# Kernel tuning notes

Hardware: AMD Instinct MI355X
Metric: run time of the kernel (lower is better)

Reference implementation:

```python
import jax, jax.numpy as jnp
import numpy as np

NUM_HEADS = 16
D_MODEL = 1024
HEAD_DIM = D_MODEL // NUM_HEADS
B, S = 2, 2048


def setup_inputs() -> dict:
    key = jax.random.key(0)
    ks = jax.random.split(key, 11)
    scale = 1.0 / np.sqrt(D_MODEL)
    inp = {
        'query': jax.random.normal(ks[0], (B, S, D_MODEL), jnp.float32),
        'key': jax.random.normal(ks[1], (B, S, D_MODEL), jnp.float32),
        'value': jax.random.normal(ks[2], (B, S, D_MODEL), jnp.float32),
        'Wq': jax.random.normal(ks[3], (D_MODEL, D_MODEL), jnp.float32) * scale,
        'bq': jnp.zeros((D_MODEL,), jnp.float32),
        'Wk': jax.random.normal(ks[4], (D_MODEL, D_MODEL), jnp.float32) * scale,
        'bk': jnp.zeros((D_MODEL,), jnp.float32),
        'Wv': jax.random.normal(ks[5], (D_MODEL, D_MODEL), jnp.float32) * scale,
        'bv': jnp.zeros((D_MODEL,), jnp.float32),
        'Wo': jax.random.normal(ks[6], (D_MODEL, D_MODEL), jnp.float32) * scale,
        'bo': jnp.zeros((D_MODEL,), jnp.float32),
    }
    return inp


def reference(query, key, value, Wq, bq, Wk, bk, Wv, bv, Wo, bo):
    b, s, _ = query.shape
    # Linear projections (torch Linear: x @ W.T + b; here W stored as [in,out])
    Q = query @ Wq + bq
    K = key @ Wk + bk
    V = value @ Wv + bv
    # [B, H, S, Dh]
    Q = Q.reshape(b, s, NUM_HEADS, HEAD_DIM).transpose(0, 2, 1, 3)
    K = K.reshape(b, -1, NUM_HEADS, HEAD_DIM).transpose(0, 2, 1, 3)
    V = V.reshape(b, -1, NUM_HEADS, HEAD_DIM).transpose(0, 2, 1, 3)
    scores = jnp.einsum('bhqd,bhkd->bhqk', Q, K) / jnp.sqrt(jnp.float32(HEAD_DIM)).astype(Q.dtype)
    attn = jax.nn.softmax(scores, axis=-1)
    ctx = jnp.einsum('bhqk,bhkd->bhqd', attn, V)
    ctx = ctx.transpose(0, 2, 1, 3).reshape(b, s, D_MODEL)
    return ctx @ Wo + bo
```

## Files before the change

kernel.cpp:

```cpp
#include <hip/hip_runtime.h>
#include <hip/hip_bf16.h>
#include <math.h>

#define NUM_HEADS 16
#define D_MODEL 1024
#define HEAD_DIM 64
#define BATCH 2
#define SEQ 2048
#define M_TOTAL (BATCH*SEQ)

typedef __bf16 bf16;
typedef __bf16 bf16x2 __attribute__((ext_vector_type(2)));
typedef __bf16 bf16x4 __attribute__((ext_vector_type(4)));
typedef __bf16 bf16x8 __attribute__((ext_vector_type(8)));
typedef float  floatx4  __attribute__((ext_vector_type(4)));
typedef float  floatx16 __attribute__((ext_vector_type(16)));
typedef unsigned int uintx2 __attribute__((ext_vector_type(2)));
typedef unsigned int uintx4 __attribute__((ext_vector_type(4)));

#define CLSCALE 0.180336884f

#if __has_builtin(__builtin_amdgcn_exp2f)
#define EXP2(x) __builtin_amdgcn_exp2f(x)
#else
#define EXP2(x) exp2f(x)
#endif

__device__ __forceinline__ void async_copy16(const bf16* g, bf16* l) {
    __builtin_amdgcn_global_load_lds(
        (const __attribute__((address_space(1))) void*)g,
        (__attribute__((address_space(3))) void*)l, 16, 0, 0);
}

__device__ __forceinline__ unsigned pk2(float lo, float hi) {
    bf16x2 t; t[0] = (bf16)lo; t[1] = (bf16)hi;
    return __builtin_bit_cast(unsigned, t);
}

__global__ __launch_bounds__(256)
void convert_kernel(const float* __restrict__ Wq, const float* __restrict__ Wk,
                    const float* __restrict__ Wv, const float* __restrict__ Wo,
                    const float* __restrict__ q, const float* __restrict__ k,
                    const float* __restrict__ v,
                    bf16* __restrict__ Wt, bf16* __restrict__ Xb)
{
    const int blk = blockIdx.x;
    const int tid = threadIdx.x;
    if (blk < 256) {
        const int wi  = blk >> 6;
        const int sub = blk & 63;
        const int xb  = sub & 3;
        const int yb  = sub >> 2;
        const float* W = (wi == 0) ? Wq : (wi == 1) ? Wk : (wi == 2) ? Wv : Wo;
        bf16* dstM = Wt + (size_t)wi * D_MODEL * D_MODEL;
        const int n  = xb * 256 + tid;
        const int k0 = yb * 64;
        bf16* dst = dstM + (size_t)n * D_MODEL + k0;
        #pragma unroll
        for (int jc = 0; jc < 8; ++jc) {
            bf16x8 w;
            #pragma unroll
            for (int j = 0; j < 8; ++j)
                w[j] = (bf16)W[(size_t)(k0 + jc * 8 + j) * D_MODEL + n];
            *(bf16x8*)(dst + jc * 8) = w;
        }
    } else {
        const int rem   = blk - 256;
        const int plane = rem >> 11;
        const int xb    = rem & 2047;
        const float* X = (plane == 0) ? q : (plane == 1) ? k : v;
        bf16* dst = Xb + (size_t)plane * M_TOTAL * D_MODEL;
        size_t i = ((size_t)xb * 256 + tid) * 8;
        const float4 u = *(const float4*)(X + i);
        const float4 w = *(const float4*)(X + i + 4);
        bf16x8 o;
        o[0] = (bf16)u.x; o[1] = (bf16)u.y; o[2] = (bf16)u.z; o[3] = (bf16)u.w;
        o[4] = (bf16)w.x; o[5] = (bf16)w.y; o[6] = (bf16)w.z; o[7] = (bf16)w.w;
        *(bf16x8*)(dst + i) = o;
    }
}

__global__ __launch_bounds__(256)
void proj_kernel(const bf16* __restrict__ Xb, const bf16* __restrict__ Wt,
                 const float* __restrict__ bq, const float* __restrict__ bk,
                 const float* __restrict__ bv,
                 bf16* __restrict__ Qo, bf16* __restrict__ Ko, bf16* __restrict__ Vto)
{
    const int lin  = blockIdx.x;
    const int xcd  = lin & 7;
    const int idx  = lin >> 3;
    const int nt   = idx & 7;
    const int t2   = idx >> 3;
    const int mloc = t2 & 3;
    const int which= t2 >> 2;
    const int tileM = (xcd * 4 + mloc) * 128;
    const int tileN = nt * 128;

    const bf16* X     = Xb + (size_t)which * M_TOTAL * D_MODEL;
    const bf16* Wm    = Wt + (size_t)which * D_MODEL * D_MODEL;
    const float* bias = (which == 0) ? bq : (which == 1) ? bk : bv;

    const int tid  = threadIdx.x;
    const int lane = tid & 63;
    const int wave = tid >> 6;
    const int quad = lane >> 4;
    const int l16  = lane & 15;

    __shared__ bf16 sA[128 * 32];
    __shared__ bf16 sB[128 * 32];

    floatx4 acc[4][4];
    const floatx4 z4 = {0.0f, 0.0f, 0.0f, 0.0f};
    #pragma unroll
    for (int i = 0; i < 4; i++)
        #pragma unroll
        for (int j = 0; j < 4; j++) acc[i][j] = z4;

    const int wm = (wave >> 1) * 64;
    const int wn = (wave & 1) * 64;

    const int c0   = wave * 64 + lane;
    const int row0 = c0 >> 2, col0 = (c0 & 3) * 8;
    const int c1   = c0 + 256;
    const int row1 = c1 >> 2, col1 = (c1 & 3) * 8;
    bf16* ldsA0 = sA + (size_t)(wave * 64) * 8;
    bf16* ldsA1 = sA + (size_t)(256 + wave * 64) * 8;
    bf16* ldsB0 = sB + (size_t)(wave * 64) * 8;
    bf16* ldsB1 = sB + (size_t)(256 + wave * 64) * 8;

    for (int k0 = 0; k0 < D_MODEL; k0 += 32) {
        __syncthreads();
        async_copy16(X  + (size_t)(tileM + row0) * D_MODEL + k0 + col0, ldsA0);
        async_copy16(X  + (size_t)(tileM + row1) * D_MODEL + k0 + col1, ldsA1);
        async_copy16(Wm + (size_t)(tileN + row0) * D_MODEL + k0 + col0, ldsB0);
        async_copy16(Wm + (size_t)(tileN + row1) * D_MODEL + k0 + col1, ldsB1);
        __syncthreads();

        bf16x8 af[4], bfr[4];
        #pragma unroll
        for (int i = 0; i < 4; i++) af[i]  = *(const bf16x8*)&sA[(wm + i * 16 + l16) * 32 + quad * 8];
        #pragma unroll
        for (int j = 0; j < 4; j++) bfr[j] = *(const bf16x8*)&sB[(wn + j * 16 + l16) * 32 + quad * 8];
        if (which != 2) {
            #pragma unroll
            for (int i = 0; i < 4; i++)
                #pragma unroll
                for (int j = 0; j < 4; j++)
                    acc[i][j] = __builtin_amdgcn_mfma_f32_16x16x32_bf16(af[i], bfr[j], acc[i][j], 0, 0, 0);
        } else {
            #pragma unroll
            for (int i = 0; i < 4; i++)
                #pragma unroll
                for (int j = 0; j < 4; j++)
                    acc[i][j] = __builtin_amdgcn_mfma_f32_16x16x32_bf16(bfr[i], af[j], acc[i][j], 0, 0, 0);
        }
    }

    if (which != 2) {
        bf16* out = (which == 0) ? Qo : Ko;
        const float oscale = (which == 0) ? CLSCALE : 1.0f;
        #pragma unroll
        for (int i = 0; i < 4; i++) {
            int mbase = tileM + wm + i * 16 + quad * 4;
            #pragma unroll
            for (int j = 0; j < 4; j++) {
                int n = tileN + wn + j * 16 + l16;
                float bb = bias[n];
                int h = n >> 6, d = n & 63;
                #pragma unroll
                for (int r = 0; r < 4; r++) {
                    int mm = mbase + r;
                    int b = mm >> 11, s = mm & 2047;
                    out[(((size_t)(b * NUM_HEADS + h)) * SEQ + s) * HEAD_DIM + d] =
                        (bf16)((acc[i][j][r] + bb) * oscale);
                }
            }
        }
    } else {
        #pragma unroll
        for (int i = 0; i < 4; i++) {
            #pragma unroll
            for (int r = 0; r < 4; r++) {
                int n = tileN + wn + i * 16 + quad * 4 + r;
                float bb = bias[n];
                int h = n >> 6, d = n & 63;
                #pragma unroll
                for (int j = 0; j < 4; j++) {
                    int m = tileM + wm + j * 16 + l16;
                    int b = m >> 11, s = m & 2047;
                    Vto[(((size_t)(b * NUM_HEADS + h)) * HEAD_DIM + d) * SEQ + s] =
                        (bf16)(acc[i][j][r] + bb);
                }
            }
        }
    }
}

__global__ __launch_bounds__(256)
void attn_kernel(const bf16* __restrict__ Q, const bf16* __restrict__ K,
                 const bf16* __restrict__ Vt, bf16* __restrict__ Ctx)
{
    const int lin    = blockIdx.x;
    const int xcd    = lin & 7;
    const int rest   = lin >> 3;
    const int superg = rest >> 5;
    const int qi     = rest & 31;
    const int bh     = superg * 8 + xcd;
    const int b      = bh >> 4, h = bh & 15;
    const int q0     = qi * 64;

    const int tid  = threadIdx.x;
    const int lane = tid & 63;
    const int wave = tid >> 6;
    const int half = lane >> 5;
    const int m31  = lane & 31;
    const int xs   = m31 & 7;

    const int qsub  = wave & 1;
    const int kjsub = wave >> 1;

    __shared__ bf16 sK[2][64 * 64];
    __shared__ bf16 sV[2][64 * 64];
    __shared__ float sL[64];

    const bf16* Qb  = Q  + ((size_t)bh * SEQ + q0) * HEAD_DIM;
    const bf16* Kb  = K  + (size_t)bh * SEQ * HEAD_DIM;
    const bf16* Vtb = Vt + (size_t)bh * HEAD_DIM * SEQ;

    bf16x8 bQ[4];
    #pragma unroll
    for (int s = 0; s < 4; s++)
        bQ[s] = *(const bf16x8*)(Qb + (size_t)(qsub * 32 + m31) * HEAD_DIM + s * 16 + half * 8);

    #pragma unroll
    for (int it = 0; it < 2; ++it) {
        int c    = tid + it * 256;
        int row  = c >> 3;
        int scol = ((c & 7) ^ (row & 7)) * 8;
        async_copy16(Kb  + (size_t)row * HEAD_DIM + scol, &sK[0][c * 8]);
        async_copy16(Vtb + (size_t)row * SEQ + scol,      &sV[0][c * 8]);
    }

    floatx16 o0, o1;
    #pragma unroll
    for (int r = 0; r < 16; r++) { o0[r] = 0.0f; o1[r] = 0.0f; }
    float lp = 0.0f;

    for (int kt = 0; kt < SEQ / 64; ++kt) {
        const int p = kt & 1;
        __syncthreads();

        bf16x8 aK[4];
        #pragma unroll
        for (int s = 0; s < 4; s++)
            aK[s] = *(const bf16x8*)&sK[p][(kjsub * 32 + m31) * 64 + (((2 * s + half) ^ xs) * 8)];

        if (kt + 1 < SEQ / 64) {
            #pragma unroll
            for (int it = 0; it < 2; ++it) {
                int c    = tid + it * 256;
                int row  = c >> 3;
                int scol = ((c & 7) ^ (row & 7)) * 8;
                async_copy16(Kb  + (size_t)((kt + 1) * 64 + row) * HEAD_DIM + scol,
                             &sK[p ^ 1][c * 8]);
                async_copy16(Vtb + (size_t)row * SEQ + (kt + 1) * 64 + scol,
                             &sV[p ^ 1][c * 8]);
            }
        }

        floatx16 sc;
        #pragma unroll
        for (int r = 0; r < 16; r++) sc[r] = 0.0f;
        __builtin_amdgcn_s_setprio(1);
        #pragma unroll
        for (int s = 0; s < 4; s++)
            sc = __builtin_amdgcn_mfma_f32_32x32x16_bf16(aK[s], bQ[s], sc, 0, 0, 0);
        __builtin_amdgcn_s_setprio(0);

        #pragma unroll
        for (int r = 0; r < 16; r++) sc[r] = EXP2(sc[r]);
        float ls = 0.0f;
        #pragma unroll
        for (int r = 0; r < 16; r++) ls += sc[r];
        lp += ls;

        bf16x8 bP[2];
        #pragma unroll
        for (int s = 0; s < 2; s++) {
            const int bs = 8 * s;
            unsigned x = pk2(sc[bs + 0], sc[bs + 1]);
            unsigned z = pk2(sc[bs + 2], sc[bs + 3]);
            unsigned y = pk2(sc[bs + 4], sc[bs + 5]);
            unsigned w = pk2(sc[bs + 6], sc[bs + 7]);
            auto r0 = __builtin_amdgcn_permlane32_swap(x, y, false, false);
            auto r1 = __builtin_amdgcn_permlane32_swap(z, w, false, false);
            uintx4 bp;
            bp[0] = r0[0]; bp[1] = r1[0]; bp[2] = r0[1]; bp[3] = r1[1];
            bP[s] = __builtin_bit_cast(bf16x8, bp);
        }

        __builtin_amdgcn_s_setprio(1);
        #pragma unroll
        for (int s = 0; s < 2; s++) {
            int ch = ((4 * kjsub + 2 * s + half) ^ xs) * 8;
            bf16x8 a0 = *(const bf16x8*)&sV[p][(size_t)m31 * 64 + ch];
            bf16x8 a1 = *(const bf16x8*)&sV[p][(size_t)(32 + m31) * 64 + ch];
            o0 = __builtin_amdgcn_mfma_f32_32x32x16_bf16(a0, bP[s], o0, 0, 0, 0);
            o1 = __builtin_amdgcn_mfma_f32_32x32x16_bf16(a1, bP[s], o1, 0, 0, 0);
        }
        __builtin_amdgcn_s_setprio(0);
    }

    lp += __shfl_xor(lp, 32, 64);

    __syncthreads();
    float* fO = (qsub == 0) ? (float*)&sK[0][0] : (float*)&sK[1][0];
    if (kjsub == 1) {
        #pragma unroll
        for (int r = 0; r < 16; r++) {
            fO[r * 64 + lane]        = o0[r];
            fO[1024 + r * 64 + lane] = o1[r];
        }
        if (half == 0) sL[qsub * 32 + m31] = lp;
    }
    __syncthreads();
    if (kjsub == 0) {
        #pragma unroll
        for (int r = 0; r < 16; r++) {
            o0[r] += fO[r * 64 + lane];
            o1[r] += fO[1024 + r * 64 + lane];
        }
        float denom = lp + sL[qsub * 32 + m31];
        float inv = 1.0f / denom;

        int q = q0 + qsub * 32 + m31;
        size_t base = ((size_t)b * SEQ + q) * D_MODEL + h * HEAD_DIM;
        #pragma unroll
        for (int rg = 0; rg < 4; rg++) {
            int d0 = rg * 8 + half * 4;
            bf16x4 w0, w1;
            #pragma unroll
            for (int i = 0; i < 4; i++) {
                w0[i] = (bf16)(o0[rg * 4 + i] * inv);
                w1[i] = (bf16)(o1[rg * 4 + i] * inv);
            }
            *(bf16x4*)&Ctx[base + d0]      = w0;
            *(bf16x4*)&Ctx[base + 32 + d0] = w1;
        }
    }
}

__global__ __launch_bounds__(256)
void out_proj_kernel(const bf16* __restrict__ A, const bf16* __restrict__ Wto,
                     const float* __restrict__ bias, float* __restrict__ Out)
{
    const int lin  = blockIdx.x;
    const int xcd  = lin & 7;
    const int idx  = lin >> 3;
    const int nt   = idx & 7;
    const int mloc = idx >> 3;
    const int tileM = (xcd * 8 + mloc) * 64;
    const int tileN = nt * 128;

    const int tid  = threadIdx.x;
    const int lane = tid & 63;
    const int wave = tid >> 6;
    const int quad = lane >> 4;
    const int l16  = lane & 15;

    __shared__ bf16 sA[64 * 32];
    __shared__ bf16 sB[128 * 32];

    floatx4 acc[2][4];
    const floatx4 z4 = {0.0f, 0.0f, 0.0f, 0.0f};
    #pragma unroll
    for (int i = 0; i < 2; i++)
        #pragma unroll
        for (int j = 0; j < 4; j++) acc[i][j] = z4;

    const int wm = (wave >> 1) * 32;
    const int wn = (wave & 1) * 64;

    const int c0   = wave * 64 + lane;
    const int row0 = c0 >> 2, col0 = (c0 & 3) * 8;
    const int c1   = c0 + 256;
    const int row1 = c1 >> 2, col1 = (c1 & 3) * 8;
    bf16* ldsA0 = sA + (size_t)(wave * 64) * 8;
    bf16* ldsB0 = sB + (size_t)(wave * 64) * 8;
    bf16* ldsB1 = sB + (size_t)(256 + wave * 64) * 8;

    for (int k0 = 0; k0 < D_MODEL; k0 += 32) {
        __syncthreads();
        async_copy16(A   + (size_t)(tileM + row0) * D_MODEL + k0 + col0, ldsA0);
        async_copy16(Wto + (size_t)(tileN + row0) * D_MODEL + k0 + col0, ldsB0);
        async_copy16(Wto + (size_t)(tileN + row1) * D_MODEL + k0 + col1, ldsB1);
        __syncthreads();

        bf16x8 af[2], bfr[4];
        #pragma unroll
        for (int i = 0; i < 2; i++) af[i]  = *(const bf16x8*)&sA[(wm + i * 16 + l16) * 32 + quad * 8];
        #pragma unroll
        for (int j = 0; j < 4; j++) bfr[j] = *(const bf16x8*)&sB[(wn + j * 16 + l16) * 32 + quad * 8];
        #pragma unroll
        for (int i = 0; i < 2; i++)
            #pragma unroll
            for (int j = 0; j < 4; j++)
                acc[i][j] = __builtin_amdgcn_mfma_f32_16x16x32_bf16(af[i], bfr[j], acc[i][j], 0, 0, 0);
    }

    #pragma unroll
    for (int i = 0; i < 2; i++) {
        int mbase = tileM + wm + i * 16 + quad * 4;
        #pragma unroll
        for (int j = 0; j < 4; j++) {
            int n = tileN + wn + j * 16 + l16;
            float bb = bias[n];
            #pragma unroll
            for (int r = 0; r < 4; r++)
                Out[(size_t)(mbase + r) * D_MODEL + n] = acc[i][j][r] + bb;
        }
    }
}

extern "C" void kernel_launch(void* const* d_in, const int* in_sizes, int n_in,
                              void* d_out, int out_size, void* d_ws, size_t ws_size,
                              hipStream_t stream)
{
    const float* q  = (const float*)d_in[0];
    const float* k  = (const float*)d_in[1];
    const float* v  = (const float*)d_in[2];
    const float* Wq = (const float*)d_in[3];
    const float* bq = (const float*)d_in[4];
    const float* Wk = (const float*)d_in[5];
    const float* bk = (const float*)d_in[6];
    const float* Wv = (const float*)d_in[7];
    const float* bv = (const float*)d_in[8];
    const float* Wo = (const float*)d_in[9];
    const float* bo = (const float*)d_in[10];
    float* out = (float*)d_out;

    const size_t PLANE = (size_t)M_TOTAL * D_MODEL;
    bf16* Qb = (bf16*)d_ws;
    bf16* Kb = Qb + PLANE;
    bf16* Vt = Kb + PLANE;
    bf16* Cb = Vt + PLANE;
    bf16* Wt = Cb + PLANE;
    bf16* Xb = Wt + 4 * (size_t)D_MODEL * D_MODEL;

    convert_kernel<<<dim3(6400), 256, 0, stream>>>(Wq, Wk, Wv, Wo, q, k, v, Wt, Xb);
    proj_kernel<<<dim3(768), 256, 0, stream>>>(Xb, Wt, bq, bk, bv, Qb, Kb, Vt);
    attn_kernel<<<dim3(1024), 256, 0, stream>>>(Qb, Kb, Vt, Cb);
    out_proj_kernel<<<dim3(512), 256, 0, stream>>>(Cb, Wt + 3 * (size_t)D_MODEL * D_MODEL, bo, out);
}
```

Before: 236.9 us.

## Double-buffer LDS tiles and use fragment-ordered layout in projection GEMMs

Both the QKV projection kernel and the output projection kernel now use two LDS buffers. The next K-slice is prefetched with async copies while MFMAs run on the current slice, which removes one barrier per iteration and overlaps global loads with compute. The LDS tiles are also stored in fragment order, so each lane reads 16 contiguous bytes and bank conflicts are avoided. In exchange, LDS use per block doubles, which may reduce occupancy.

Result: slower. 254.4 us (+7.4%).

```diff
diff --git a/kernel.cpp b/kernel.cpp
--- a/kernel.cpp
+++ b/kernel.cpp
@@ -106,8 +106,8 @@
     const int quad = lane >> 4;
     const int l16  = lane & 15;
 
-    __shared__ bf16 sA[128 * 32];
-    __shared__ bf16 sB[128 * 32];
+    __shared__ bf16 sA[2][4096];
+    __shared__ bf16 sB[2][4096];
 
     floatx4 acc[4][4];
     const floatx4 z4 = {0.0f, 0.0f, 0.0f, 0.0f};
@@ -116,31 +116,39 @@
         #pragma unroll
         for (int j = 0; j < 4; j++) acc[i][j] = z4;
 
-    const int wm = (wave >> 1) * 64;
-    const int wn = (wave & 1) * 64;
-
-    const int c0   = wave * 64 + lane;
-    const int row0 = c0 >> 2, col0 = (c0 & 3) * 8;
-    const int c1   = c0 + 256;
-    const int row1 = c1 >> 2, col1 = (c1 & 3) * 8;
-    bf16* ldsA0 = sA + (size_t)(wave * 64) * 8;
-    bf16* ldsA1 = sA + (size_t)(256 + wave * 64) * 8;
-    bf16* ldsB0 = sB + (size_t)(wave * 64) * 8;
-    bf16* ldsB1 = sB + (size_t)(256 + wave * 64) * 8;
-
-    for (int k0 = 0; k0 < D_MODEL; k0 += 32) {
+    const int rC = ((tid >> 6) & 3) * 16 + (tid & 15);
+    const int cC = ((tid >> 4) & 3) * 8;
+    const bf16* gA0 = X  + (size_t)(tileM + rC) * D_MODEL + cC;
+    const bf16* gA1 = gA0 + (size_t)64 * D_MODEL;
+    const bf16* gB0 = Wm + (size_t)(tileN + rC) * D_MODEL + cC;
+    const bf16* gB1 = gB0 + (size_t)64 * D_MODEL;
+
+    async_copy16(gA0, &sA[0][tid * 8]);
+    async_copy16(gA1, &sA[0][(tid + 256) * 8]);
+    async_copy16(gB0, &sB[0][tid * 8]);
+    async_copy16(gB1, &sB[0][(tid + 256) * 8]);
+
+    const int fA = (wave >> 1) * 4;
+    const int fB = (wave & 1) * 4;
+
+    for (int kt = 0; kt < 32; ++kt) {
+        const int p = kt & 1;
         __syncthreads();
-        async_copy16(X  + (size_t)(tileM + row0) * D_MODEL + k0 + col0, ldsA0);
-        async_copy16(X  + (size_t)(tileM + row1) * D_MODEL + k0 + col1, ldsA1);
-        async_copy16(Wm + (size_t)(tileN + row0) * D_MODEL + k0 + col0, ldsB0);
-        async_copy16(Wm + (size_t)(tileN + row1) * D_MODEL + k0 + col1, ldsB1);
-        __syncthreads();
 
         bf16x8 af[4], bfr[4];
         #pragma unroll
-        for (int i = 0; i < 4; i++) af[i]  = *(const bf16x8*)&sA[(wm + i * 16 + l16) * 32 + quad * 8];
-        #pragma unroll
-        for (int j = 0; j < 4; j++) bfr[j] = *(const bf16x8*)&sB[(wn + j * 16 + l16) * 32 + quad * 8];
+        for (int i = 0; i < 4; i++) af[i]  = *(const bf16x8*)&sA[p][((fA + i) * 64 + lane) * 8];
+        #pragma unroll
+        for (int j = 0; j < 4; j++) bfr[j] = *(const bf16x8*)&sB[p][((fB + j) * 64 + lane) * 8];
+
+        if (kt < 31) {
+            const int k0 = (kt + 1) * 32;
+            async_copy16(gA0 + k0, &sA[p ^ 1][tid * 8]);
+            async_copy16(gA1 + k0, &sA[p ^ 1][(tid + 256) * 8]);
+            async_copy16(gB0 + k0, &sB[p ^ 1][tid * 8]);
+            async_copy16(gB1 + k0, &sB[p ^ 1][(tid + 256) * 8]);
+        }
+
         if (which != 2) {
             #pragma unroll
             for (int i = 0; i < 4; i++)
@@ -155,6 +163,9 @@
                     acc[i][j] = __builtin_amdgcn_mfma_f32_16x16x32_bf16(bfr[i], af[j], acc[i][j], 0, 0, 0);
         }
     }
+
+    const int wm = (wave >> 1) * 64;
+    const int wn = (wave & 1) * 64;
 
     if (which != 2) {
         bf16* out = (which == 0) ? Qo : Ko;
@@ -368,8 +379,8 @@
     const int quad = lane >> 4;
     const int l16  = lane & 15;
 
-    __shared__ bf16 sA[64 * 32];
-    __shared__ bf16 sB[128 * 32];
+    __shared__ bf16 sA[2][2048];
+    __shared__ bf16 sB[2][4096];
 
     floatx4 acc[2][4];
     const floatx4 z4 = {0.0f, 0.0f, 0.0f, 0.0f};
@@ -378,35 +389,46 @@
         #pragma unroll
         for (int j = 0; j < 4; j++) acc[i][j] = z4;
 
+    const int rA = ((tid >> 7) & 1) * 32 + ((tid >> 6) & 1) * 16 + (tid & 15);
+    const int rB = ((tid >> 6) & 3) * 16 + (tid & 15);
+    const int cC = ((tid >> 4) & 3) * 8;
+    const bf16* gA0 = A   + (size_t)(tileM + rA) * D_MODEL + cC;
+    const bf16* gB0 = Wto + (size_t)(tileN + rB) * D_MODEL + cC;
+    const bf16* gB1 = gB0 + (size_t)64 * D_MODEL;
+
+    async_copy16(gA0, &sA[0][tid * 8]);
+    async_copy16(gB0, &sB[0][tid * 8]);
+    async_copy16(gB1, &sB[0][(tid + 256) * 8]);
+
+    const int fA = (wave >> 1) * 2;
+    const int fB = (wave & 1) * 4;
+
+    for (int kt = 0; kt < 32; ++kt) {
+        const int p = kt & 1;
+        __syncthreads();
+
+        bf16x8 af[2], bfr[4];
+        #pragma unroll
+        for (int i = 0; i < 2; i++) af[i]  = *(const bf16x8*)&sA[p][((fA + i) * 64 + lane) * 8];
+        #pragma unroll
+        for (int j = 0; j < 4; j++) bfr[j] = *(const bf16x8*)&sB[p][((fB + j) * 64 + lane) * 8];
+
+        if (kt < 31) {
+            const int k0 = (kt + 1) * 32;
+            async_copy16(gA0 + k0, &sA[p ^ 1][tid * 8]);
+            async_copy16(gB0 + k0, &sB[p ^ 1][tid * 8]);
+            async_copy16(gB1 + k0, &sB[p ^ 1][(tid + 256) * 8]);
+        }
+
+        #pragma unroll
+        for (int i = 0; i < 2; i++)
+            #pragma unroll
+            for (int j = 0; j < 4; j++)
+                acc[i][j] = __builtin_amdgcn_mfma_f32_16x16x32_bf16(af[i], bfr[j], acc[i][j], 0, 0, 0);
+    }
+
     const int wm = (wave >> 1) * 32;
     const int wn = (wave & 1) * 64;
-
-    const int c0   = wave * 64 + lane;
-    const int row0 = c0 >> 2, col0 = (c0 & 3) * 8;
-    const int c1   = c0 + 256;
-    const int row1 = c1 >> 2, col1 = (c1 & 3) * 8;
-    bf16* ldsA0 = sA + (size_t)(wave * 64) * 8;
-    bf16* ldsB0 = sB + (size_t)(wave * 64) * 8;
-    bf16* ldsB1 = sB + (size_t)(256 + wave * 64) * 8;
-
-    for (int k0 = 0; k0 < D_MODEL; k0 += 32) {
-        __syncthreads();
-        async_copy16(A   + (size_t)(tileM + row0) * D_MODEL + k0 + col0, ldsA0);
-        async_copy16(Wto + (size_t)(tileN + row0) * D_MODEL + k0 + col0, ldsB0);
-        async_copy16(Wto + (size_t)(tileN + row1) * D_MODEL + k0 + col1, ldsB1);
-        __syncthreads();
-
-        bf16x8 af[2], bfr[4];
-        #pragma unroll
-        for (int i = 0; i < 2; i++) af[i]  = *(const bf16x8*)&sA[(wm + i * 16 + l16) * 32 + quad * 8];
-        #pragma unroll
-        for (int j = 0; j < 4; j++) bfr[j] = *(const bf16x8*)&sB[(wn + j * 16 + l16) * 32 + quad * 8];
-        #pragma unroll
-        for (int i = 0; i < 2; i++)
-            #pragma unroll
-            for (int j = 0; j < 4; j++)
-                acc[i][j] = __builtin_amdgcn_mfma_f32_16x16x32_bf16(af[i], bfr[j], acc[i][j], 0, 0, 0);
-    }
 
     #pragma unroll
     for (int i = 0; i < 2; i++) {
```

## Use fragment-ordered LDS layout and K=64 tiles in projection GEMMs

Applied to the files above, without the earlier changes.

The QKV projection and output projection kernels now stage 64-wide K slices instead of 32, which halves the number of barrier pairs per tile. Global-to-LDS async copies are remapped so that LDS holds data already in MFMA fragment order. Each lane then reads its bf16x8 fragment from a contiguous lane-indexed slot, which is meant to avoid LDS bank conflicts from the old row-major 32-wide layout. LDS use per block doubles, which may reduce occupancy, and the copies are still not double-buffered.

New measurement: 257.8 us. 8.8% more time.

```diff
diff --git a/kernel.cpp b/kernel.cpp
--- a/kernel.cpp
+++ b/kernel.cpp
@@ -15,7 +15,6 @@
 typedef __bf16 bf16x8 __attribute__((ext_vector_type(8)));
 typedef float  floatx4  __attribute__((ext_vector_type(4)));
 typedef float  floatx16 __attribute__((ext_vector_type(16)));
-typedef unsigned int uintx2 __attribute__((ext_vector_type(2)));
 typedef unsigned int uintx4 __attribute__((ext_vector_type(4)));
 
 #define CLSCALE 0.180336884f
@@ -106,8 +105,8 @@
     const int quad = lane >> 4;
     const int l16  = lane & 15;
 
-    __shared__ bf16 sA[128 * 32];
-    __shared__ bf16 sB[128 * 32];
+    __shared__ bf16 sA[16 * 64 * 8];
+    __shared__ bf16 sB[16 * 64 * 8];
 
     floatx4 acc[4][4];
     const floatx4 z4 = {0.0f, 0.0f, 0.0f, 0.0f};
@@ -116,45 +115,54 @@
         #pragma unroll
         for (int j = 0; j < 4; j++) acc[i][j] = z4;
 
+    const int row0 = ((tid >> 7) & 1) * 16 + (tid & 15);
+    const int colC = ((tid >> 6) & 1) * 32 + ((tid >> 4) & 3) * 8;
+    const bf16* gA = X  + (size_t)(tileM + row0) * D_MODEL + colC;
+    const bf16* gB = Wm + (size_t)(tileN + row0) * D_MODEL + colC;
+
+    const int fA = (wave >> 1) * 4;
+    const int fB = (wave & 1) * 4;
+
+    for (int kt = 0; kt < 16; ++kt) {
+        const int k0 = kt * 64;
+        __syncthreads();
+
+        #pragma unroll
+        for (int it = 0; it < 4; ++it) {
+            async_copy16(gA + (size_t)(32 * it) * D_MODEL + k0, &sA[(tid + 256 * it) * 8]);
+            async_copy16(gB + (size_t)(32 * it) * D_MODEL + k0, &sB[(tid + 256 * it) * 8]);
+        }
+
+        __syncthreads();
+
+        #pragma unroll
+        for (int ks = 0; ks < 2; ++ks) {
+            bf16x8 af[4], bfr[4];
+            #pragma unroll
+            for (int i = 0; i < 4; i++)
+                af[i]  = *(const bf16x8*)&sA[(((fA + i) * 2 + ks) * 64 + lane) * 8];
+            #pragma unroll
+            for (int j = 0; j < 4; j++)
+                bfr[j] = *(const bf16x8*)&sB[(((fB + j) * 2 + ks) * 64 + lane) * 8];
+
+            if (which != 2) {
+                #pragma unroll
+                for (int i = 0; i < 4; i++)
+                    #pragma unroll
+                    for (int j = 0; j < 4; j++)
+                        acc[i][j] = __builtin_amdgcn_mfma_f32_16x16x32_bf16(af[i], bfr[j], acc[i][j], 0, 0, 0);
+            } else {
+                #pragma unroll
+                for (int i = 0; i < 4; i++)
+                    #pragma unroll
+                    for (int j = 0; j < 4; j++)
+                        acc[i][j] = __builtin_amdgcn_mfma_f32_16x16x32_bf16(bfr[i], af[j], acc[i][j], 0, 0, 0);
+            }
+        }
+    }
+
     const int wm = (wave >> 1) * 64;
     const int wn = (wave & 1) * 64;
-
-    const int c0   = wave * 64 + lane;
-    const int row0 = c0 >> 2, col0 = (c0 & 3) * 8;
-    const int c1   = c0 + 256;
-    const int row1 = c1 >> 2, col1 = (c1 & 3) * 8;
-    bf16* ldsA0 = sA + (size_t)(wave * 64) * 8;
-    bf16* ldsA1 = sA + (size_t)(256 + wave * 64) * 8;
-    bf16* ldsB0 = sB + (size_t)(wave * 64) * 8;
-    bf16* ldsB1 = sB + (size_t)(256 + wave * 64) * 8;
-
-    for (int k0 = 0; k0 < D_MODEL; k0 += 32) {
-        __syncthreads();
-        async_copy16(X  + (size_t)(tileM + row0) * D_MODEL + k0 + col0, ldsA0);
-        async_copy16(X  + (size_t)(tileM + row1) * D_MODEL + k0 + col1, ldsA1);
-        async_copy16(Wm + (size_t)(tileN + row0) * D_MODEL + k0 + col0, ldsB0);
-        async_copy16(Wm + (size_t)(tileN + row1) * D_MODEL + k0 + col1, ldsB1);
-        __syncthreads();
-
-        bf16x8 af[4], bfr[4];
-        #pragma unroll
-        for (int i = 0; i < 4; i++) af[i]  = *(const bf16x8*)&sA[(wm + i * 16 + l16) * 32 + quad * 8];
-        #pragma unroll
-        for (int j = 0; j < 4; j++) bfr[j] = *(const bf16x8*)&sB[(wn + j * 16 + l16) * 32 + quad * 8];
-        if (which != 2) {
-            #pragma unroll
-            for (int i = 0; i < 4; i++)
-                #pragma unroll
-                for (int j = 0; j < 4; j++)
-                    acc[i][j] = __builtin_amdgcn_mfma_f32_16x16x32_bf16(af[i], bfr[j], acc[i][j], 0, 0, 0);
-        } else {
-            #pragma unroll
-            for (int i = 0; i < 4; i++)
-                #pragma unroll
-                for (int j = 0; j < 4; j++)
-                    acc[i][j] = __builtin_amdgcn_mfma_f32_16x16x32_bf16(bfr[i], af[j], acc[i][j], 0, 0, 0);
-        }
-    }
 
     if (which != 2) {
         bf16* out = (which == 0) ? Qo : Ko;
@@ -368,8 +376,8 @@
     const int quad = lane >> 4;
     const int l16  = lane & 15;
 
-    __shared__ bf16 sA[64 * 32];
-    __shared__ bf16 sB[128 * 32];
+    __shared__ bf16 sA[8 * 64 * 8];
+    __shared__ bf16 sB[16 * 64 * 8];
 
     floatx4 acc[2][4];
     const floatx4 z4 = {0.0f, 0.0f, 0.0f, 0.0f};
@@ -378,35 +386,46 @@
         #pragma unroll
         for (int j = 0; j < 4; j++) acc[i][j] = z4;
 
+    const int row0 = ((tid >> 7) & 1) * 16 + (tid & 15);
+    const int colC = ((tid >> 6) & 1) * 32 + ((tid >> 4) & 3) * 8;
+    const bf16* gA = A   + (size_t)(tileM + row0) * D_MODEL + colC;
+    const bf16* gB = Wto + (size_t)(tileN + row0) * D_MODEL + colC;
+
+    const int fA = (wave >> 1) * 2;
+    const int fB = (wave & 1) * 4;
+
+    for (int kt = 0; kt < 16; ++kt) {
+        const int k0 = kt * 64;
+        __syncthreads();
+
+        async_copy16(gA + k0,                            &sA[tid * 8]);
+        async_copy16(gA + (size_t)32 * D_MODEL + k0,     &sA[(tid + 256) * 8]);
+        #pragma unroll
+        for (int it = 0; it < 4; ++it)
+            async_copy16(gB + (size_t)(32 * it) * D_MODEL + k0, &sB[(tid + 256 * it) * 8]);
+
+        __syncthreads();
+
+        #pragma unroll
+        for (int ks = 0; ks < 2; ++ks) {
+            bf16x8 af[2], bfr[4];
+            #pragma unroll
+            for (int i = 0; i < 2; i++)
+                af[i]  = *(const bf16x8*)&sA[(((fA + i) * 2 + ks) * 64 + lane) * 8];
+            #pragma unroll
+            for (int j = 0; j < 4; j++)
+                bfr[j] = *(const bf16x8*)&sB[(((fB + j) * 2 + ks) * 64 + lane) * 8];
+
+            #pragma unroll
+            for (int i = 0; i < 2; i++)
+                #pragma unroll
+                for (int j = 0; j < 4; j++)
+                    acc[i][j] = __builtin_amdgcn_mfma_f32_16x16x32_bf16(af[i], bfr[j], acc[i][j], 0, 0, 0);
+        }
+    }
+
     const int wm = (wave >> 1) * 32;
     const int wn = (wave & 1) * 64;
-
-    const int c0   = wave * 64 + lane;
-    const int row0 = c0 >> 2, col0 = (c0 & 3) * 8;
-    const int c1   = c0 + 256;
-    const int row1 = c1 >> 2, col1 = (c1 & 3) * 8;
-    bf16* ldsA0 = sA + (size_t)(wave * 64) * 8;
-    bf16* ldsB0 = sB + (size_t)(wave * 64) * 8;
-    bf16* ldsB1 = sB + (size_t)(256 + wave * 64) * 8;
-
-    for (int k0 = 0; k0 < D_MODEL; k0 += 32) {
-        __syncthreads();
-        async_copy16(A   + (size_t)(tileM + row0) * D_MODEL + k0 + col0, ldsA0);
-        async_copy16(Wto + (size_t)(tileN + row0) * D_MODEL + k0 + col0, ldsB0);
-        async_copy16(Wto + (size_t)(tileN + row1) * D_MODEL + k0 + col1, ldsB1);
-        __syncthreads();
-
-        bf16x8 af[2], bfr[4];
-        #pragma unroll
-        for (int i = 0; i < 2; i++) af[i]  = *(const bf16x8*)&sA[(wm + i * 16 + l16) * 32 + quad * 8];
-        #pragma unroll
-        for (int j = 0; j < 4; j++) bfr[j] = *(const bf16x8*)&sB[(wn + j * 16 + l16) * 32 + quad * 8];
-        #pragma unroll
-        for (int i = 0; i < 2; i++)
-            #pragma unroll
-            for (int j = 0; j < 4; j++)
-                acc[i][j] = __builtin_amdgcn_mfma_f32_16x16x32_bf16(af[i], bfr[j], acc[i][j], 0, 0, 0);
-    }
 
     #pragma unroll
     for (int i = 0; i < 2; i++) {
```
